# Optimization experiments

Measured on AMD Instinct MI355X. Metric: run time of the kernel, lower is better.

The kernel has to match this reference:

```python
import jax, jax.numpy as jnp
import numpy as np

B, C, H, W = 4, 96, 64, 64
N_STATE, DT_RANK, K = 16, 6, 3


def _layernorm(x, g, b, eps=1e-5):
    m = jnp.mean(x, axis=-1, keepdims=True)
    v = jnp.mean((x - m) ** 2, axis=-1, keepdims=True)
    return (x - m) / jnp.sqrt(v + eps) * g + b


def _grid_sample(img, gx, gy):
    # F.grid_sample: bilinear, align_corners=True, zeros padding; gx,gy in [-1,1], [B,Ho,Wo]
    Bc, Cc, Hi, Wi = img.shape
    fx = (gx + 1.0) * 0.5 * (Wi - 1)
    fy = (gy + 1.0) * 0.5 * (Hi - 1)
    x0 = jnp.floor(fx)
    y0 = jnp.floor(fy)
    wx1 = fx - x0
    wy1 = fy - y0

    def tap(ix, iy, w):
        valid = ((ix >= 0) & (ix < Wi) & (iy >= 0) & (iy < Hi)).astype(img.dtype)
        ic = jnp.clip(ix, 0, Wi - 1).astype(jnp.int32)
        jc = jnp.clip(iy, 0, Hi - 1).astype(jnp.int32)
        v = jax.vmap(lambda im, yy, xx: im[:, yy, xx])(img, jc, ic)  # [B,C,Ho,Wo]
        return v * (w * valid)[:, None, :, :]

    return (tap(x0, y0, (1 - wx1) * (1 - wy1)) + tap(x0 + 1, y0, wx1 * (1 - wy1))
            + tap(x0, y0 + 1, (1 - wx1) * wy1) + tap(x0 + 1, y0 + 1, wx1 * wy1))


def _resize_bilinear(img, Ho, Wo):
    # torch F.interpolate(mode='bilinear', align_corners=False)
    Bc, Cc, Hi, Wi = img.shape

    def src(n_out, n_in):
        s = jnp.maximum((jnp.arange(n_out, dtype=img.dtype) + 0.5) * (n_in / n_out) - 0.5, 0.0)
        i0 = jnp.floor(s).astype(jnp.int32)
        i1 = jnp.minimum(i0 + 1, n_in - 1)
        return i0, i1, s - i0

    y0, y1, wy = src(Ho, Hi)
    x0, x1, wx = src(Wo, Wi)
    row = img[:, :, y0, :] * (1 - wy)[None, None, :, None] + img[:, :, y1, :] * wy[None, None, :, None]
    return row[:, :, :, x0] * (1 - wx) + row[:, :, :, x1] * wx


def _conv_offset(x, conv1_w, conv1_b, ca1_w, ca1_b, ca2_w, ca2_b, ln_g, ln_b, conv2_w):
    Bc, Cc = x.shape[:2]
    p = conv1_w.shape[-1] // 2
    x1 = jax.lax.conv_general_dilated(
        x, conv1_w, (1, 1), [(p, p), (p, p)],
        dimension_numbers=("NCHW", "OIHW", "NCHW"), feature_group_count=Cc
    ) + conv1_b[None, :, None, None]
    xc = jnp.mean(x, axis=(2, 3))  # adaptive_avg_pool2d -> (1,1)
    hid = jax.nn.gelu(xc @ ca1_w.T + ca1_b, approximate=False)
    ca = jax.nn.sigmoid(hid @ ca2_w.T + ca2_b)
    x1 = x1 * ca[:, :, None, None]
    xn = _layernorm(jnp.transpose(x1, (0, 2, 3, 1)), ln_g, ln_b)
    xg = jax.nn.gelu(jnp.transpose(xn, (0, 3, 1, 2)), approximate=False)
    return jnp.einsum("bchw,oc->bohw", xg, conv2_w[:, :, 0, 0])


def _deformable(x, rpe_table, conv1_w, conv1_b, ca1_w, ca1_b, ca2_w, ca2_b, ln_g, ln_b, conv2_w):
    Bc, Cc, Hc, Wc = x.shape
    L = Hc * Wc
    off = _conv_offset(x, conv1_w, conv1_b, ca1_w, ca1_b, ca2_w, ca2_b, ln_g, ln_b, conv2_w)
    offset = off[:, :2]
    de = off[:, 2]
    rng = jnp.array([1.0 / (Hc - 1.0), 1.0 / (Wc - 1.0)], off.dtype).reshape(1, 2, 1, 1)
    offset = jnp.transpose(jnp.tanh(offset) * rng, (0, 2, 3, 1))  # [B,H,W,2] (dy,dx)
    ry = (jnp.linspace(0.5, Hc - 0.5, Hc) / (Hc - 1.0)) * 2.0 - 1.0
    rx = (jnp.linspace(0.5, Wc - 0.5, Wc) / (Wc - 1.0)) * 2.0 - 1.0
    ref = jnp.stack(jnp.meshgrid(ry, rx, indexing="ij"), -1)  # [H,W,2] (y,x)
    pos = offset + ref[None]
    de_index = jnp.tanh(de).reshape(Bc, L)
    path_ref = (jnp.linspace(0.5, L - 0.5, L) / (L - 1.0)) * 2.0 - 1.0
    path_pos = de_index + path_ref[None]
    x_sampled = _grid_sample(x, pos[..., 1], pos[..., 0])
    rpe = jnp.broadcast_to(rpe_table[None], (Bc,) + rpe_table.shape)
    rpe_bias = _resize_bilinear(rpe, Hc, Wc)
    ky = (jnp.linspace(0.0, float(Hc), Hc) / (Hc - 1.0)) * 2.0 - 1.0
    kx = (jnp.linspace(0.0, float(Wc), Wc) / (Wc - 1.0)) * 2.0 - 1.0
    key_grid = jnp.stack(jnp.meshgrid(ky, kx, indexing="ij"), -1)
    disp = (key_grid[None] - pos) * 0.5
    pos_bias = _grid_sample(rpe_bias, disp[..., 1], disp[..., 0])
    xd = (x_sampled + pos_bias).reshape(Bc, Cc, L)
    indices = jnp.argsort(path_pos, axis=-1)  # topk(k=N, largest=False) == ascending argsort
    xs2 = jnp.take_along_axis(xd, indices[:, None, :], axis=2)
    return xs2, indices


def _selective_scan(u, delta, A, Bs, Cs, Dv, delta_bias):
    Bc, KD, L = u.shape
    Kk = Bs.shape[1]
    Dd = KD // Kk
    Ns = A.shape[1]
    delta = jax.nn.softplus(delta + delta_bias[None, :, None])
    dt4 = jnp.moveaxis(delta.reshape(Bc, Kk, Dd, L), 3, 0)
    u4 = jnp.moveaxis(u.reshape(Bc, Kk, Dd, L), 3, 0)
    Bt = jnp.moveaxis(Bs, 3, 0)
    Ct = jnp.moveaxis(Cs, 3, 0)
    A3 = A.reshape(Kk, Dd, Ns)

    @jax.checkpoint
    def step(h, inp):
        dt, ut, bt, ct = inp  # [B,K,D],[B,K,D],[B,K,N],[B,K,N]
        h = jnp.exp(dt[..., None] * A3) * h + (dt * ut)[..., None] * bt[:, :, None, :]
        return h, jnp.einsum("bkdn,bkn->bkd", h, ct)

    h0 = jnp.zeros((Bc, Kk, Dd, Ns), u.dtype)
    _, ys = jax.lax.scan(step, h0, (dt4, u4, Bt, Ct))
    ys = jnp.moveaxis(ys, 0, 3).reshape(Bc, KD, L)
    return ys + u * Dv[None, :, None]


def _forward(x, x_proj_weight, dt_projs_weight, dt_projs_bias, A_logs, Ds_param,
             conv1_w, conv1_b, ca1_w, ca1_b, ca2_w, ca2_b, ln_g, ln_b, conv2_w, rpe_table):
    Bc, Dd, Hc, Wc = x.shape
    L = Hc * Wc
    Kk, _, R = dt_projs_weight.shape
    Ns = A_logs.shape[1]
    xs0 = x.reshape(Bc, Dd, L)
    xs2, indices = _deformable(x, rpe_table, conv1_w, conv1_b, ca1_w, ca1_b, ca2_w, ca2_b, ln_g, ln_b, conv2_w)
    xs = jnp.stack([xs0, xs0[..., ::-1], xs2], axis=1)  # [B,3,D,L]
    x_dbl = jnp.einsum("bkdl,kcd->bkcl", xs, x_proj_weight)
    dts, Bs, Cs = jnp.split(x_dbl, [R, R + Ns], axis=2)
    dts = jnp.einsum("bkrl,kdr->bkdl", dts, dt_projs_weight)
    A = -jnp.exp(A_logs)
    ys = _selective_scan(xs.reshape(Bc, Kk * Dd, L), dts.reshape(Bc, Kk * Dd, L),
                         A, Bs, Cs, Ds_param, dt_projs_bias.reshape(-1))
    ys = ys.reshape(Bc, Kk, Dd, L)
    inv = jnp.argsort(indices, axis=-1)  # inverse permutation (DeformableLayerReverse)
    y2 = jnp.take_along_axis(ys[:, 2], inv[:, None, :], axis=2)
    y = (ys[:, 0] + ys[:, 1][..., ::-1] + y2) / 3.0
    return jnp.transpose(y, (0, 2, 1)).reshape(Bc, Hc, Wc, Dd)


def setup_inputs():
    key = jax.random.key(0)
    ks = jax.random.split(key, 12)
    f = jnp.float32
    return {
        "x": jax.random.normal(ks[0], (B, C, H, W), f),
        "x_proj_weight": jax.random.normal(ks[1], (K, DT_RANK + 2 * N_STATE, C), f) * 0.05,
        "dt_projs_weight": jax.random.normal(ks[2], (K, C, DT_RANK), f) * 0.05,
        "dt_projs_bias": jax.random.normal(ks[3], (K, C), f) * 0.1,
        "A_logs": jnp.tile(jnp.log(jnp.arange(1, N_STATE + 1, dtype=f))[None, :], (K * C, 1)),
        "Ds_param": jnp.ones((K * C,), f),
        "conv1_w": jax.random.normal(ks[4], (C, 1, 9, 9), f) * 0.05,
        "conv1_b": jnp.zeros((C,), f),
        "ca1_w": jax.random.normal(ks[5], (C // 16, C), f) * 0.1,
        "ca1_b": jnp.zeros((C // 16,), f),
        "ca2_w": jax.random.normal(ks[6], (C, C // 16), f) * 0.1,
        "ca2_b": jnp.zeros((C,), f),
        "ln_g": jnp.ones((C,), f),
        "ln_b": jnp.zeros((C,), f),
        "conv2_w": jax.random.normal(ks[7], (3, C, 1, 1), f) * 0.05,
        "rpe_table": jax.random.normal(ks[8], (C, 7, 7), f) * 0.01,
    }


def reference(x, x_proj_weight, dt_projs_weight, dt_projs_bias, A_logs, Ds_param,
              conv1_w, conv1_b, ca1_w, ca1_b, ca2_w, ca2_b, ln_g, ln_b, conv2_w, rpe_table):
    return _forward(x, x_proj_weight, dt_projs_weight, dt_projs_bias, A_logs, Ds_param,
                    conv1_w, conv1_b, ca1_w, ca1_b, ca2_w, ca2_b, ln_g, ln_b, conv2_w, rpe_table)
```

## Files before the change

kernel.cpp:

```cpp
#include <hip/hip_runtime.h>

#define BB 4
#define CC 96
#define HH 64
#define WW 64
#define LL 4096
#define KK 3
#define RR 6
#define NN 16

__device__ __forceinline__ float geluf(float x){
    return 0.5f * x * (1.0f + erff(x * 0.70710678118654752f));
}
__device__ __forceinline__ float softplusf(float x){
    return fmaxf(x, 0.0f) + log1pf(expf(-fabsf(x)));
}
__device__ __forceinline__ float sigmoidf(float x){
    return 1.0f / (1.0f + expf(-x));
}

__global__ __launch_bounds__(256) void k_mean(const float* __restrict__ x, float* __restrict__ xc){
    int bc = blockIdx.x;
    const float* p = x + (size_t)bc * LL;
    float s = 0.f;
    for (int i = threadIdx.x; i < LL; i += 256) s += p[i];
    __shared__ float red[256];
    red[threadIdx.x] = s; __syncthreads();
    for (int st = 128; st > 0; st >>= 1){
        if (threadIdx.x < st) red[threadIdx.x] += red[threadIdx.x + st];
        __syncthreads();
    }
    if (threadIdx.x == 0) xc[bc] = red[0] * (1.0f / LL);
}

__global__ __launch_bounds__(128) void k_ca(const float* __restrict__ xc,
                     const float* __restrict__ w1, const float* __restrict__ b1,
                     const float* __restrict__ w2, const float* __restrict__ b2,
                     float* __restrict__ ca){
    int b = blockIdx.x;
    int t = threadIdx.x;
    __shared__ float hid[CC/16];
    if (t < CC/16){
        float a = b1[t];
        for (int d = 0; d < CC; d++) a += w1[t*CC + d] * xc[b*CC + d];
        hid[t] = geluf(a);
    }
    __syncthreads();
    if (t < CC){
        float a = b2[t];
        #pragma unroll
        for (int i = 0; i < CC/16; i++) a += w2[t*(CC/16) + i] * hid[i];
        ca[b*CC + t] = sigmoidf(a);
    }
}

__global__ __launch_bounds__(256) void k_conv(const float* __restrict__ x, const float* __restrict__ w,
                       const float* __restrict__ bias, const float* __restrict__ ca,
                       float* __restrict__ x1){
    int tid4 = blockIdx.x * 256 + threadIdx.x;
    int wq4 = (tid4 & 15) * 4;
    int rest = tid4 >> 4;
    int h = rest & 63;
    int bc = rest >> 6;
    int c = bc % CC; int b = bc / CC;
    const float* xp = x + (size_t)bc * LL;
    const float* wp = w + c * 81;
    float a0 = 0.f, a1 = 0.f, a2 = 0.f, a3 = 0.f;
    #pragma unroll
    for (int ky = 0; ky < 9; ky++){
        int yy = h + ky - 4;
        if (yy < 0 || yy >= HH) continue;
        const float4* row4 = (const float4*)(xp + yy*WW);
        int g = wq4 >> 2;
        float4 q0 = (wq4 >= 4)  ? row4[g-1] : make_float4(0.f,0.f,0.f,0.f);
        float4 q1 = row4[g];
        float4 q2 = (wq4 < 60)  ? row4[g+1] : make_float4(0.f,0.f,0.f,0.f);
        float v[12] = {q0.x,q0.y,q0.z,q0.w, q1.x,q1.y,q1.z,q1.w, q2.x,q2.y,q2.z,q2.w};
        const float* wr = wp + ky*9;
        #pragma unroll
        for (int kx = 0; kx < 9; kx++){
            float wk = wr[kx];
            a0 = fmaf(v[kx],   wk, a0);
            a1 = fmaf(v[kx+1], wk, a1);
            a2 = fmaf(v[kx+2], wk, a2);
            a3 = fmaf(v[kx+3], wk, a3);
        }
    }
    float sc = ca[b*CC + c];
    float bb = bias[c];
    float4 o = make_float4((a0+bb)*sc, (a1+bb)*sc, (a2+bb)*sc, (a3+bb)*sc);
    *(float4*)(x1 + (size_t)bc*LL + h*WW + wq4) = o;
}

__global__ __launch_bounds__(256) void k_rpe(const float* __restrict__ t, float* __restrict__ out){
    int gid = blockIdx.x * 256 + threadIdx.x;
    int l = gid & (LL-1); int c = gid >> 12;
    int h = l >> 6, w = l & 63;
    float sy = fmaxf((h + 0.5f) * (7.0f/64.0f) - 0.5f, 0.f);
    float sx = fmaxf((w + 0.5f) * (7.0f/64.0f) - 0.5f, 0.f);
    int y0 = (int)floorf(sy); int x0 = (int)floorf(sx);
    float wy = sy - (float)y0, wx = sx - (float)x0;
    int y1 = min(y0 + 1, 6), x1i = min(x0 + 1, 6);
    const float* tp = t + c * 49;
    float r0 = tp[y0*7 + x0] * (1.f - wy) + tp[y1*7 + x0] * wy;
    float r1 = tp[y0*7 + x1i] * (1.f - wy) + tp[y1*7 + x1i] * wy;
    out[gid] = r0 * (1.f - wx) + r1 * wx;
}

__global__ __launch_bounds__(256) void k_off(const float* __restrict__ x1,
                      const float* __restrict__ g, const float* __restrict__ bta,
                      const float* __restrict__ w2,
                      float* __restrict__ posy, float* __restrict__ posx, float* __restrict__ path){
    int blk = blockIdx.x;
    int ltile = blk & 63; int b = blk >> 6;
    int lane = threadIdx.x & 63;
    int wg = threadIdx.x >> 6;
    int l = ltile * 64 + lane;
    const float* p = x1 + (size_t)b * CC * LL + l;
    float v[24];
    float s = 0.f, ss = 0.f;
    #pragma unroll
    for (int j = 0; j < 24; j++){
        float t = p[(size_t)(wg*24 + j) * LL];
        v[j] = t; s += t; ss += t*t;
    }
    __shared__ float ls[4][64], lss[4][64];
    ls[wg][lane] = s; lss[wg][lane] = ss;
    __syncthreads();
    s  = ls[0][lane]  + ls[1][lane]  + ls[2][lane]  + ls[3][lane];
    ss = lss[0][lane] + lss[1][lane] + lss[2][lane] + lss[3][lane];
    float m = s * (1.0f/CC);
    float rstd = rsqrtf(ss*(1.0f/CC) - m*m + 1e-5f);
    float a0 = 0.f, a1 = 0.f, a2 = 0.f;
    #pragma unroll
    for (int j = 0; j < 24; j++){
        int c = wg*24 + j;
        float xn = (v[j]-m)*rstd*g[c] + bta[c];
        float xg = geluf(xn);
        a0 = fmaf(w2[c],      xg, a0);
        a1 = fmaf(w2[CC+c],   xg, a1);
        a2 = fmaf(w2[2*CC+c], xg, a2);
    }
    __shared__ float la[3][4][64];
    la[0][wg][lane] = a0; la[1][wg][lane] = a1; la[2][wg][lane] = a2;
    __syncthreads();
    if (wg < 3){
        float a = la[wg][0][lane] + la[wg][1][lane] + la[wg][2][lane] + la[wg][3][lane];
        int h = l >> 6, w = l & 63;
        if (wg == 0)      posy[b*LL + l] = tanhf(a)*(1.0f/63.0f) + ((2*h+1)*(1.0f/63.0f) - 1.0f);
        else if (wg == 1) posx[b*LL + l] = tanhf(a)*(1.0f/63.0f) + ((2*w+1)*(1.0f/63.0f) - 1.0f);
        else              path[b*LL + l] = tanhf(a) + ((l + 0.5f)*(2.0f/4095.0f) - 1.0f);
    }
}

__device__ __forceinline__ float bilin0(const float* __restrict__ img, float gx, float gy){
    float fx = (gx + 1.f) * 31.5f;
    float fy = (gy + 1.f) * 31.5f;
    float x0f = floorf(fx), y0f = floorf(fy);
    float wx = fx - x0f, wy = fy - y0f;
    int x0 = (int)x0f, y0 = (int)y0f;
    float acc = 0.f;
    bool vx0 = (x0 >= 0) & (x0 < WW), vx1 = (x0+1 >= 0) & (x0+1 < WW);
    bool vy0 = (y0 >= 0) & (y0 < HH), vy1 = (y0+1 >= 0) & (y0+1 < HH);
    if (vy0 & vx0) acc += img[y0*WW + x0]       * (1.f-wx) * (1.f-wy);
    if (vy0 & vx1) acc += img[y0*WW + x0+1]     * wx       * (1.f-wy);
    if (vy1 & vx0) acc += img[(y0+1)*WW + x0]   * (1.f-wx) * wy;
    if (vy1 & vx1) acc += img[(y0+1)*WW + x0+1] * wx       * wy;
    return acc;
}

typedef unsigned long long u64s;
__device__ __forceinline__ u64s shflx64(u64s x, int m){
    int lo = __shfl_xor((int)(unsigned)x, m);
    int hi = __shfl_xor((int)(unsigned)(x >> 32), m);
    return ((u64s)(unsigned)hi << 32) | (unsigned)lo;
}
__device__ __forceinline__ void cex(u64s& a, u64s& b, bool up){
    u64s mn = a < b ? a : b;
    u64s mx = a < b ? b : a;
    a = up ? mn : mx;
    b = up ? mx : mn;
}
__global__ __launch_bounds__(1024) void k_sortsample(
        const float* __restrict__ path, int* __restrict__ idx, int* __restrict__ inv,
        const float* __restrict__ x, const float* __restrict__ rpe,
        const float* __restrict__ posy, const float* __restrict__ posx,
        float* __restrict__ xd){
    int blk = blockIdx.x;
    if (blk < BB){
        int b = blk;
        int t = threadIdx.x;
        __shared__ u64s lds[LL];
        u64s v[4];
        #pragma unroll
        for (int r = 0; r < 4; r++){
            int e = t*4 + r;
            unsigned u = __float_as_uint(path[b*LL + e]);
            u ^= (u >> 31) ? 0xFFFFFFFFu : 0x80000000u;
            v[r] = ((u64s)u << 32) | (unsigned)e;
        }
        for (int kk = 2; kk <= LL; kk <<= 1){
            for (int j = kk >> 1; j > 0; j >>= 1){
                if (j >= 256){
                    __syncthreads();
                    #pragma unroll
                    for (int r = 0; r < 4; r++) lds[t*4 + r] = v[r];
                    __syncthreads();
                    #pragma unroll
                    for (int r = 0; r < 4; r++){
                        int e = t*4 + r;
                        u64s pv = lds[e ^ j];
                        bool up    = ((e & kk) == 0);
                        bool lower = ((e & j) == 0);
                        u64s mn = v[r] < pv ? v[r] : pv;
                        u64s mx = v[r] < pv ? pv : v[r];
                        v[r] = (up == lower) ? mn : mx;
                    }
                } else if (j >= 4){
                    int m = j >> 2;
                    #pragma unroll
                    for (int r = 0; r < 4; r++){
                        u64s pv = shflx64(v[r], m);
                        bool up    = (((t*4 + r) & kk) == 0);
                        bool lower = ((t & m) == 0);
                        u64s mn = v[r] < pv ? v[r] : pv;
                        u64s mx = v[r] < pv ? pv : v[r];
                        v[r] = (up == lower) ? mn : mx;
                    }
                } else if (j == 2){
                    bool up = (((t*4) & kk) == 0);
                    cex(v[0], v[2], up);
                    cex(v[1], v[3], up);
                } else {
                    if (kk == 2){
                        cex(v[0], v[1], true);
                        cex(v[2], v[3], false);
                    } else {
                        bool up = (((t*4) & kk) == 0);
                        cex(v[0], v[1], up);
                        cex(v[2], v[3], up);
                    }
                }
            }
        }
        #pragma unroll
        for (int r = 0; r < 4; r++){
            int e = t*4 + r;
            int id = (int)(unsigned)(v[r] & 0xFFFFFFFFu);
            idx[b*LL + e] = id;
            inv[b*LL + id] = e;
        }
    } else {
        int gid = (blk - BB) * 1024 + threadIdx.x;
        int l = gid & (LL-1); int bc = gid >> 12;
        int b = bc / CC; int c = bc % CC;
        float gy = posy[b*LL + l], gx = posx[b*LL + l];
        float v = bilin0(x + (size_t)bc * LL, gx, gy);
        int h = l >> 6, w = l & 63;
        float ky = h * (128.0f/3969.0f) - 1.0f;
        float kx = w * (128.0f/3969.0f) - 1.0f;
        float v2 = bilin0(rpe + (size_t)c * LL, (kx - gx) * 0.5f, (ky - gy) * 0.5f);
        xd[gid] = v + v2;
    }
}

__global__ __launch_bounds__(192, 1) void k_proj(const float* __restrict__ x, const float* __restrict__ xd,
    const int* __restrict__ indices, const float* __restrict__ xpw, const float* __restrict__ dtw,
    const float* __restrict__ dtb, float* __restrict__ u2, float* __restrict__ dt,
    float* __restrict__ Bst, float* __restrict__ Cst){
    int blk = blockIdx.x;
    int ltile = blk & 63; int bk = blk >> 6;
    int k = bk % KK; int b = bk / KK;
    int lane = threadIdx.x & 63;
    int w = threadIdx.x >> 6;
    const float* __restrict__ Wk = xpw + k*38*CC;
    int l = ltile * 64 + lane;
    int srcl = (k == 0) ? l : (k == 1 ? (LL-1-l) : indices[b*LL + l]);
    const float* xp = (k == 2 ? xd : x) + (size_t)b * CC * LL + srcl;

    __shared__ float vsh[CC*64];
    #pragma unroll
    for (int j = 0; j < 32; j++){
        int d = w*32 + j;
        vsh[d*64 + lane] = xp[(size_t)d * LL];
    }
    __syncthreads();

    if (w == 0){
        float acc[RR];
        #pragma unroll
        for (int i = 0; i < RR; i++) acc[i] = 0.f;
        for (int d = 0; d < CC; d++){
            float vv = vsh[d*64 + lane];
            #pragma unroll
            for (int i = 0; i < RR; i++) acc[i] = fmaf(Wk[i*CC + d], vv, acc[i]);
        }
        const float* __restrict__ Dw = dtw + k*CC*RR;
        const float* __restrict__ Db = dtb + k*CC;
        float* dtp = dt + (size_t)bk * CC * LL + l;
        #pragma unroll 8
        for (int d = 0; d < CC; d++){
            float sdt = Db[d];
            #pragma unroll
            for (int r = 0; r < RR; r++) sdt = fmaf(acc[r], Dw[d*RR + r], sdt);
            dtp[(size_t)d * LL] = softplusf(sdt);
        }
    } else if (w == 1){
        float acc[NN];
        #pragma unroll
        for (int i = 0; i < NN; i++) acc[i] = 0.f;
        for (int d = 0; d < CC; d++){
            float vv = vsh[d*64 + lane];
            #pragma unroll
            for (int i = 0; i < NN; i++) acc[i] = fmaf(Wk[(RR + i)*CC + d], vv, acc[i]);
        }
        size_t base = ((size_t)bk * LL + l) * NN;
        #pragma unroll
        for (int q = 0; q < 4; q++){
            float4 o; o.x = acc[q*4]; o.y = acc[q*4+1]; o.z = acc[q*4+2]; o.w = acc[q*4+3];
            *(float4*)(Bst + base + q*4) = o;
        }
    } else {
        float acc[NN];
        #pragma unroll
        for (int i = 0; i < NN; i++) acc[i] = 0.f;
        for (int d = 0; d < CC; d++){
            float vv = vsh[d*64 + lane];
            #pragma unroll
            for (int i = 0; i < NN; i++) acc[i] = fmaf(Wk[(RR + NN + i)*CC + d], vv, acc[i]);
        }
        size_t base = ((size_t)bk * LL + l) * NN;
        #pragma unroll
        for (int q = 0; q < 4; q++){
            float4 o; o.x = acc[q*4]; o.y = acc[q*4+1]; o.z = acc[q*4+2]; o.w = acc[q*4+3];
            *(float4*)(Cst + base + q*4) = o;
        }
        if (k == 2){
            float* up = u2 + (size_t)b * CC * LL + l;
            #pragma unroll 8
            for (int d = 0; d < CC; d++) up[(size_t)d * LL] = vsh[d*64 + lane];
        }
    }
}

#define SEG 128
#define TL 32
#define SROW 17
#define XROW 32
template<int KIND>
__device__ __forceinline__ void scan_body(int b, int d, const float* __restrict__ usrc,
    const float* __restrict__ dt, const float* __restrict__ Bst, const float* __restrict__ Cst,
    const float* __restrict__ Alog, const float* __restrict__ Ds, float* __restrict__ ys,
    float* sA, float* sB, float* sS, float* yl){
    int bk = b * KK + KIND;
    int tid = threadIdx.x;
    int ng = tid & 3;
    int seg = tid >> 2;
    int t0 = seg * TL;
    int xsw = (seg & 7) << 2;

    const float4 A4 = *(const float4*)(Alog + (KIND*CC + d)*NN + 4*ng);
    const float L2E = 1.4426950408889634f;
    float A2[4] = { -__expf(A4.x)*L2E, -__expf(A4.y)*L2E, -__expf(A4.z)*L2E, -__expf(A4.w)*L2E };
    float Dv = Ds[KIND*CC + d];

    const float* dtp = dt + ((size_t)bk * CC + d) * LL + t0;
    const float* ub = (KIND == 1)
        ? usrc + ((size_t)b*CC + d) * LL + (LL-4-t0)
        : usrc + ((size_t)b*CC + d) * LL + t0;
    const float* Bp = Bst + ((size_t)bk * LL + t0) * NN + 4*ng;
    const float* Cp = Cst + ((size_t)bk * LL + t0) * NN + 4*ng;
    float* yp = ys + ((size_t)bk * CC + d) * LL + t0;

    float h[4] = {0.f,0.f,0.f,0.f};
    float S = 0.f;
    for (int t = 0; t < TL; t += 4){
        float4 dq = *(const float4*)(dtp + t);
        float4 uq = (KIND == 1) ? *(const float4*)(ub - t) : *(const float4*)(ub + t);
        float4 Bq[4], Cq[4];
        #pragma unroll
        for (int i = 0; i < 4; i++){
            Bq[i] = *(const float4*)(Bp + (t+i)*NN);
            Cq[i] = *(const float4*)(Cp + (t+i)*NN);
        }
        float dd[4] = {dq.x, dq.y, dq.z, dq.w};
        float uu[4];
        if (KIND == 1){ uu[0]=uq.w; uu[1]=uq.z; uu[2]=uq.y; uu[3]=uq.x; }
        else          { uu[0]=uq.x; uu[1]=uq.y; uu[2]=uq.z; uu[3]=uq.w; }
        float sv[4], pv[4];
        #pragma unroll
        for (int i = 0; i < 4; i++){
            float du = dd[i] * uu[i];
            float bb[4] = {Bq[i].x, Bq[i].y, Bq[i].z, Bq[i].w};
            float cc[4] = {Cq[i].x, Cq[i].y, Cq[i].z, Cq[i].w};
            float p = 0.f;
            #pragma unroll
            for (int j = 0; j < 4; j++){
                float a = exp2f(dd[i] * A2[j]);
                h[j] = fmaf(a, h[j], du * bb[j]);
                p = fmaf(h[j], cc[j], p);
            }
            S += dd[i];
            sv[i] = S;
            p += __shfl_xor(p, 1);
            p += __shfl_xor(p, 2);
            pv[i] = fmaf(uu[i], Dv, p);
        }
        if (ng == 0){
            int xo = seg*XROW + (t ^ xsw);
            *(float4*)(sS + xo) = make_float4(sv[0], sv[1], sv[2], sv[3]);
            *(float4*)(yl + xo) = make_float4(pv[0], pv[1], pv[2], pv[3]);
        }
    }

    #pragma unroll
    for (int j = 0; j < 4; j++){
        sA[seg*SROW + 4*ng + j] = exp2f(A2[j] * S);
        sB[seg*SROW + 4*ng + j] = h[j];
    }
    __syncthreads();
    {
        int wv = tid >> 6;
        int lane = tid & 63;
        #pragma unroll
        for (int nn = 0; nn < 2; nn++){
            int n = 2*wv + nn;
            float a1 = sA[(2*lane)*SROW + n],   b1 = sB[(2*lane)*SROW + n];
            float a2 = sA[(2*lane+1)*SROW + n], b2 = sB[(2*lane+1)*SROW + n];
            float ca = a1 * a2;
            float cb = fmaf(a2, b1, b2);
            #pragma unroll
            for (int off = 1; off < 64; off <<= 1){
                float ta = __shfl_up(ca, off);
                float tb = __shfl_up(cb, off);
                if (lane >= off){
                    cb = fmaf(ca, tb, cb);
                    ca *= ta;
                }
            }
            float cb_prev = __shfl_up(cb, 1);
            if (lane == 0) cb_prev = 0.f;
            sA[(2*lane)*SROW + n]   = cb_prev;
            sA[(2*lane+1)*SROW + n] = fmaf(a1, cb_prev, b1);
        }
    }
    __syncthreads();
    float hc[4];
    #pragma unroll
    for (int j = 0; j < 4; j++) hc[j] = sA[seg*SROW + 4*ng + j];

    for (int t = 0; t < TL; t += 4){
        int xo = seg*XROW + (t ^ xsw);
        float4 sq = *(const float4*)(sS + xo);
        float4 Cq[4];
        #pragma unroll
        for (int i = 0; i < 4; i++) Cq[i] = *(const float4*)(Cp + (t+i)*NN);
        float sv[4] = {sq.x, sq.y, sq.z, sq.w};
        float yo[4];
        #pragma unroll
        for (int i = 0; i < 4; i++){
            float cc[4] = {Cq[i].x, Cq[i].y, Cq[i].z, Cq[i].w};
            float corr = 0.f;
            #pragma unroll
            for (int j = 0; j < 4; j++){
                float P = exp2f(sv[i] * A2[j]);
                corr = fmaf(P * hc[j], cc[j], corr);
            }
            corr += __shfl_xor(corr, 1);
            corr += __shfl_xor(corr, 2);
            yo[i] = corr;
        }
        if (ng == 0){
            float4 ylq = *(const float4*)(yl + xo);
            float4 o = make_float4(ylq.x + yo[0], ylq.y + yo[1], ylq.z + yo[2], ylq.w + yo[3]);
            *(float4*)(yp + t) = o;
        }
    }
}

__global__ __launch_bounds__(512) void k_scan_all(const float* __restrict__ x, const float* __restrict__ u2,
    const float* __restrict__ dt, const float* __restrict__ Bst, const float* __restrict__ Cst,
    const float* __restrict__ Alog, const float* __restrict__ Ds, float* __restrict__ ys){
    __shared__ float sA[SEG*SROW];
    __shared__ float sB[SEG*SROW];
    __shared__ float sS[SEG*XROW];
    __shared__ float yl[SEG*XROW];
    int blk = blockIdx.x;
    int k = blk / (BB*CC);
    int r = blk % (BB*CC);
    int d = r % CC; int b = r / CC;
    if (k == 0)      scan_body<0>(b, d, x,  dt, Bst, Cst, Alog, Ds, ys, sA, sB, sS, yl);
    else if (k == 1) scan_body<1>(b, d, x,  dt, Bst, Cst, Alog, Ds, ys, sA, sB, sS, yl);
    else             scan_body<2>(b, d, u2, dt, Bst, Cst, Alog, Ds, ys, sA, sB, sS, yl);
}

__global__ __launch_bounds__(256) void k_comb(const float* __restrict__ ys, const int* __restrict__ inv,
                                              float* __restrict__ out){
    int tile = blockIdx.x & 255; int b = blockIdx.x >> 8;
    int l0 = tile * 16;
    __shared__ float t0[CC * 17];
    __shared__ int invs[16];
    if (threadIdx.x < 16) invs[threadIdx.x] = inv[b*LL + l0 + threadIdx.x];
    __syncthreads();
    const float* y0p = ys + (size_t)(b*KK + 0) * CC * LL;
    const float* y1p = ys + (size_t)(b*KK + 1) * CC * LL;
    const float* y2p = ys + (size_t)(b*KK + 2) * CC * LL;
    #pragma unroll
    for (int it = 0; it < 6; it++){
        int e = it * 256 + threadIdx.x;
        int li = e & 15; int c = e >> 4;
        int l = l0 + li;
        float v = y0p[(size_t)c*LL + l] + y1p[(size_t)c*LL + (LL-1-l)] + y2p[(size_t)c*LL + invs[li]];
        t0[c*17 + li] = v * (1.0f/3.0f);
    }
    __syncthreads();
    #pragma unroll
    for (int it = 0; it < 6; it++){
        int e = it * 256 + threadIdx.x;
        int c = e % CC; int li = e / CC;
        out[((size_t)b*LL + l0 + li) * CC + c] = t0[c*17 + li];
    }
}

extern "C" void kernel_launch(void* const* d_in, const int* in_sizes, int n_in,
                              void* d_out, int out_size, void* d_ws, size_t ws_size,
                              hipStream_t stream){
    const float* x    = (const float*)d_in[0];
    const float* xpw  = (const float*)d_in[1];
    const float* dtw  = (const float*)d_in[2];
    const float* dtb  = (const float*)d_in[3];
    const float* Alog = (const float*)d_in[4];
    const float* Ds   = (const float*)d_in[5];
    const float* c1w  = (const float*)d_in[6];
    const float* c1b  = (const float*)d_in[7];
    const float* ca1w = (const float*)d_in[8];
    const float* ca1b = (const float*)d_in[9];
    const float* ca2w = (const float*)d_in[10];
    const float* ca2b = (const float*)d_in[11];
    const float* lng  = (const float*)d_in[12];
    const float* lnb  = (const float*)d_in[13];
    const float* c2w  = (const float*)d_in[14];
    const float* rpet = (const float*)d_in[15];
    float* out = (float*)d_out;

    float* ws   = (float*)d_ws;
    float* xc   = ws;
    float* ca   = xc + 384;
    float* x1   = ca + 384;
    float* rpe  = x1 + (size_t)BB*CC*LL;
    float* posy = rpe + (size_t)CC*LL;
    float* posx = posy + (size_t)BB*LL;
    float* path = posx + (size_t)BB*LL;
    float* xd   = path + (size_t)BB*LL;
    int*   idx  = (int*)(xd + (size_t)BB*CC*LL);
    int*   inv  = idx + (size_t)BB*LL;
    float* u2   = (float*)(inv + (size_t)BB*LL);
    float* dtA  = u2 + (size_t)BB*CC*LL;
    float* Bst  = dtA + (size_t)BB*KK*CC*LL;
    float* Cst  = Bst + (size_t)BB*KK*LL*NN;
    float* ysA  = Cst + (size_t)BB*KK*LL*NN;

    k_mean  <<<BB*CC, 256, 0, stream>>>(x, xc);
    k_ca    <<<BB, 128, 0, stream>>>(xc, ca1w, ca1b, ca2w, ca2b, ca);
    k_conv  <<<(BB*CC*LL/4)/256, 256, 0, stream>>>(x, c1w, c1b, ca, x1);
    k_rpe   <<<(CC*LL)/256, 256, 0, stream>>>(rpet, rpe);
    k_off   <<<BB*64, 256, 0, stream>>>(x1, lng, lnb, c2w, posy, posx, path);
    k_sortsample<<<BB + (BB*CC*LL)/1024, 1024, 0, stream>>>(path, idx, inv, x, rpe, posy, posx, xd);
    k_proj  <<<BB*KK*64, 192, 0, stream>>>(x, xd, idx, xpw, dtw, dtb, u2, dtA, Bst, Cst);
    k_scan_all<<<KK*BB*CC, 512, 0, stream>>>(x, u2, dtA, Bst, Cst, Alog, Ds, ysA);
    k_comb  <<<BB*256, 256, 0, stream>>>(ysA, inv, out);
}
```

Before: 295.8 us.

## Fuse mean with RPE resize, share x tile across two projection directions, retile offset kernel

Merges the channel-mean and RPE-table resize kernels into one launch, and splits the projection kernel so directions 0 and 1 share a single shared-memory load of x (k=1 writes reversed positions), while direction 2 runs separately after sorting. The offset kernel is retiled to 32 positions by 8 channel groups, doubling its block count. The intent is to cut launch count, redundant global reads of x, and improve occupancy of the offset stage, at the cost of longer serial work per block in the fused projection kernel.

```diff
diff --git a/kernel.cpp b/kernel.cpp
--- a/kernel.cpp
+++ b/kernel.cpp
@@ -19,18 +19,34 @@
     return 1.0f / (1.0f + expf(-x));
 }
 
-__global__ __launch_bounds__(256) void k_mean(const float* __restrict__ x, float* __restrict__ xc){
-    int bc = blockIdx.x;
-    const float* p = x + (size_t)bc * LL;
-    float s = 0.f;
-    for (int i = threadIdx.x; i < LL; i += 256) s += p[i];
-    __shared__ float red[256];
-    red[threadIdx.x] = s; __syncthreads();
-    for (int st = 128; st > 0; st >>= 1){
-        if (threadIdx.x < st) red[threadIdx.x] += red[threadIdx.x + st];
-        __syncthreads();
-    }
-    if (threadIdx.x == 0) xc[bc] = red[0] * (1.0f / LL);
+__global__ __launch_bounds__(256) void k_meanrpe(const float* __restrict__ x, float* __restrict__ xc,
+                                                 const float* __restrict__ rpet, float* __restrict__ rpe){
+    int blk = blockIdx.x;
+    if (blk < BB*CC){
+        const float* p = x + (size_t)blk * LL;
+        float s = 0.f;
+        for (int i = threadIdx.x; i < LL; i += 256) s += p[i];
+        __shared__ float red[256];
+        red[threadIdx.x] = s; __syncthreads();
+        for (int st = 128; st > 0; st >>= 1){
+            if (threadIdx.x < st) red[threadIdx.x] += red[threadIdx.x + st];
+            __syncthreads();
+        }
+        if (threadIdx.x == 0) xc[blk] = red[0] * (1.0f / LL);
+    } else {
+        int gid = (blk - BB*CC) * 256 + threadIdx.x;
+        int l = gid & (LL-1); int c = gid >> 12;
+        int h = l >> 6, w = l & 63;
+        float sy = fmaxf((h + 0.5f) * (7.0f/64.0f) - 0.5f, 0.f);
+        float sx = fmaxf((w + 0.5f) * (7.0f/64.0f) - 0.5f, 0.f);
+        int y0 = (int)floorf(sy); int x0 = (int)floorf(sx);
+        float wy = sy - (float)y0, wx = sx - (float)x0;
+        int y1 = min(y0 + 1, 6), x1i = min(x0 + 1, 6);
+        const float* tp = rpet + c * 49;
+        float r0 = tp[y0*7 + x0] * (1.f - wy) + tp[y1*7 + x0] * wy;
+        float r1 = tp[y0*7 + x1i] * (1.f - wy) + tp[y1*7 + x1i] * wy;
+        rpe[gid] = r0 * (1.f - wx) + r1 * wx;
+    }
 }
 
 __global__ __launch_bounds__(128) void k_ca(const float* __restrict__ xc,
@@ -92,63 +108,51 @@
     *(float4*)(x1 + (size_t)bc*LL + h*WW + wq4) = o;
 }
 
-__global__ __launch_bounds__(256) void k_rpe(const float* __restrict__ t, float* __restrict__ out){
-    int gid = blockIdx.x * 256 + threadIdx.x;
-    int l = gid & (LL-1); int c = gid >> 12;
-    int h = l >> 6, w = l & 63;
-    float sy = fmaxf((h + 0.5f) * (7.0f/64.0f) - 0.5f, 0.f);
-    float sx = fmaxf((w + 0.5f) * (7.0f/64.0f) - 0.5f, 0.f);
-    int y0 = (int)floorf(sy); int x0 = (int)floorf(sx);
-    float wy = sy - (float)y0, wx = sx - (float)x0;
-    int y1 = min(y0 + 1, 6), x1i = min(x0 + 1, 6);
-    const float* tp = t + c * 49;
-    float r0 = tp[y0*7 + x0] * (1.f - wy) + tp[y1*7 + x0] * wy;
-    float r1 = tp[y0*7 + x1i] * (1.f - wy) + tp[y1*7 + x1i] * wy;
-    out[gid] = r0 * (1.f - wx) + r1 * wx;
-}
-
 __global__ __launch_bounds__(256) void k_off(const float* __restrict__ x1,
                       const float* __restrict__ g, const float* __restrict__ bta,
                       const float* __restrict__ w2,
                       float* __restrict__ posy, float* __restrict__ posx, float* __restrict__ path){
     int blk = blockIdx.x;
-    int ltile = blk & 63; int b = blk >> 6;
-    int lane = threadIdx.x & 63;
-    int wg = threadIdx.x >> 6;
-    int l = ltile * 64 + lane;
+    int tile = blk & 127; int b = blk >> 7;
+    int li = threadIdx.x & 31;
+    int cg = threadIdx.x >> 5;
+    int l = tile * 32 + li;
     const float* p = x1 + (size_t)b * CC * LL + l;
-    float v[24];
+    float v[12];
     float s = 0.f, ss = 0.f;
     #pragma unroll
-    for (int j = 0; j < 24; j++){
-        float t = p[(size_t)(wg*24 + j) * LL];
+    for (int j = 0; j < 12; j++){
+        float t = p[(size_t)(cg*12 + j) * LL];
         v[j] = t; s += t; ss += t*t;
     }
-    __shared__ float ls[4][64], lss[4][64];
-    ls[wg][lane] = s; lss[wg][lane] = ss;
-    __syncthreads();
-    s  = ls[0][lane]  + ls[1][lane]  + ls[2][lane]  + ls[3][lane];
-    ss = lss[0][lane] + lss[1][lane] + lss[2][lane] + lss[3][lane];
+    __shared__ float ls[8][32], lss[8][32];
+    ls[cg][li] = s; lss[cg][li] = ss;
+    __syncthreads();
+    s = 0.f; ss = 0.f;
+    #pragma unroll
+    for (int g2 = 0; g2 < 8; g2++){ s += ls[g2][li]; ss += lss[g2][li]; }
     float m = s * (1.0f/CC);
     float rstd = rsqrtf(ss*(1.0f/CC) - m*m + 1e-5f);
     float a0 = 0.f, a1 = 0.f, a2 = 0.f;
     #pragma unroll
-    for (int j = 0; j < 24; j++){
-        int c = wg*24 + j;
+    for (int j = 0; j < 12; j++){
+        int c = cg*12 + j;
         float xn = (v[j]-m)*rstd*g[c] + bta[c];
         float xg = geluf(xn);
         a0 = fmaf(w2[c],      xg, a0);
         a1 = fmaf(w2[CC+c],   xg, a1);
         a2 = fmaf(w2[2*CC+c], xg, a2);
     }
-    __shared__ float la[3][4][64];
-    la[0][wg][lane] = a0; la[1][wg][lane] = a1; la[2][wg][lane] = a2;
-    __syncthreads();
-    if (wg < 3){
-        float a = la[wg][0][lane] + la[wg][1][lane] + la[wg][2][lane] + la[wg][3][lane];
-        int h = l >> 6, w = l & 63;
-        if (wg == 0)      posy[b*LL + l] = tanhf(a)*(1.0f/63.0f) + ((2*h+1)*(1.0f/63.0f) - 1.0f);
-        else if (wg == 1) posx[b*LL + l] = tanhf(a)*(1.0f/63.0f) + ((2*w+1)*(1.0f/63.0f) - 1.0f);
+    __shared__ float la[3][8][32];
+    la[0][cg][li] = a0; la[1][cg][li] = a1; la[2][cg][li] = a2;
+    __syncthreads();
+    if (cg < 3){
+        float a = 0.f;
+        #pragma unroll
+        for (int g2 = 0; g2 < 8; g2++) a += la[cg][g2][li];
+        int h = l >> 6, ww = l & 63;
+        if (cg == 0)      posy[b*LL + l] = tanhf(a)*(1.0f/63.0f) + ((2*h+1)*(1.0f/63.0f) - 1.0f);
+        else if (cg == 1) posx[b*LL + l] = tanhf(a)*(1.0f/63.0f) + ((2*ww+1)*(1.0f/63.0f) - 1.0f);
         else              path[b*LL + l] = tanhf(a) + ((l + 0.5f)*(2.0f/4095.0f) - 1.0f);
     }
 }
@@ -264,19 +268,96 @@
     }
 }
 
-__global__ __launch_bounds__(192, 1) void k_proj(const float* __restrict__ x, const float* __restrict__ xd,
+__global__ __launch_bounds__(192, 1) void k_proj01(const float* __restrict__ x,
+    const float* __restrict__ xpw, const float* __restrict__ dtw,
+    const float* __restrict__ dtb, float* __restrict__ dt,
+    float* __restrict__ Bst, float* __restrict__ Cst){
+    int blk = blockIdx.x;
+    int ltile = blk & 63; int b = blk >> 6;
+    int lane = threadIdx.x & 63;
+    int w = threadIdx.x >> 6;
+    int l = ltile * 64 + lane;
+    const float* xp = x + (size_t)b * CC * LL + l;
+
+    __shared__ float vsh[CC*64];
+    #pragma unroll
+    for (int j = 0; j < 32; j++){
+        int d = w*32 + j;
+        vsh[d*64 + lane] = xp[(size_t)d * LL];
+    }
+    __syncthreads();
+
+    #pragma unroll
+    for (int kk = 0; kk < 2; kk++){
+        const float* __restrict__ Wk = xpw + kk*38*CC;
+        int bk = b * KK + kk;
+        int lk = (kk == 0) ? l : (LL-1-l);
+        if (w == 0){
+            float acc[RR];
+            #pragma unroll
+            for (int i = 0; i < RR; i++) acc[i] = 0.f;
+            for (int d = 0; d < CC; d++){
+                float vv = vsh[d*64 + lane];
+                #pragma unroll
+                for (int i = 0; i < RR; i++) acc[i] = fmaf(Wk[i*CC + d], vv, acc[i]);
+            }
+            const float* __restrict__ Dw = dtw + kk*CC*RR;
+            const float* __restrict__ Db = dtb + kk*CC;
+            float* dtp = dt + (size_t)bk * CC * LL + lk;
+            #pragma unroll 8
+            for (int d = 0; d < CC; d++){
+                float sdt = Db[d];
+                #pragma unroll
+                for (int r = 0; r < RR; r++) sdt = fmaf(acc[r], Dw[d*RR + r], sdt);
+                dtp[(size_t)d * LL] = softplusf(sdt);
+            }
+        } else if (w == 1){
+            float acc[NN];
+            #pragma unroll
+            for (int i = 0; i < NN; i++) acc[i] = 0.f;
+            for (int d = 0; d < CC; d++){
+                float vv = vsh[d*64 + lane];
+                #pragma unroll
+                for (int i = 0; i < NN; i++) acc[i] = fmaf(Wk[(RR + i)*CC + d], vv, acc[i]);
+            }
+            size_t base = ((size_t)bk * LL + lk) * NN;
+            #pragma unroll
+            for (int q = 0; q < 4; q++){
+                float4 o; o.x = acc[q*4]; o.y = acc[q*4+1]; o.z = acc[q*4+2]; o.w = acc[q*4+3];
+                *(float4*)(Bst + base + q*4) = o;
+            }
+        } else {
+            float acc[NN];
+            #pragma unroll
+            for (int i = 0; i < NN; i++) acc[i] = 0.f;
+            for (int d = 0; d < CC; d++){
+                float vv = vsh[d*64 + lane];
+                #pragma unroll
+                for (int i = 0; i < NN; i++) acc[i] = fmaf(Wk[(RR + NN + i)*CC + d], vv, acc[i]);
+            }
+            size_t base = ((size_t)bk * LL + lk) * NN;
+            #pragma unroll
+            for (int q = 0; q < 4; q++){
+                float4 o; o.x = acc[q*4]; o.y = acc[q*4+1]; o.z = acc[q*4+2]; o.w = acc[q*4+3];
+                *(float4*)(Cst + base + q*4) = o;
+            }
+        }
+    }
+}
+
+__global__ __launch_bounds__(192, 1) void k_proj2(const float* __restrict__ xd,
     const int* __restrict__ indices, const float* __restrict__ xpw, const float* __restrict__ dtw,
     const float* __restrict__ dtb, float* __restrict__ u2, float* __restrict__ dt,
     float* __restrict__ Bst, float* __restrict__ Cst){
     int blk = blockIdx.x;
-    int ltile = blk & 63; int bk = blk >> 6;
-    int k = bk % KK; int b = bk / KK;
+    int ltile = blk & 63; int b = blk >> 6;
     int lane = threadIdx.x & 63;
     int w = threadIdx.x >> 6;
-    const float* __restrict__ Wk = xpw + k*38*CC;
+    const float* __restrict__ Wk = xpw + 2*38*CC;
+    int bk = b * KK + 2;
     int l = ltile * 64 + lane;
-    int srcl = (k == 0) ? l : (k == 1 ? (LL-1-l) : indices[b*LL + l]);
-    const float* xp = (k == 2 ? xd : x) + (size_t)b * CC * LL + srcl;
+    int srcl = indices[b*LL + l];
+    const float* xp = xd + (size_t)b * CC * LL + srcl;
 
     __shared__ float vsh[CC*64];
     #pragma unroll
@@ -295,8 +376,8 @@
             #pragma unroll
             for (int i = 0; i < RR; i++) acc[i] = fmaf(Wk[i*CC + d], vv, acc[i]);
         }
-        const float* __restrict__ Dw = dtw + k*CC*RR;
-        const float* __restrict__ Db = dtb + k*CC;
+        const float* __restrict__ Dw = dtw + 2*CC*RR;
+        const float* __restrict__ Db = dtb + 2*CC;
         float* dtp = dt + (size_t)bk * CC * LL + l;
         #pragma unroll 8
         for (int d = 0; d < CC; d++){
@@ -335,11 +416,9 @@
             float4 o; o.x = acc[q*4]; o.y = acc[q*4+1]; o.z = acc[q*4+2]; o.w = acc[q*4+3];
             *(float4*)(Cst + base + q*4) = o;
         }
-        if (k == 2){
-            float* up = u2 + (size_t)b * CC * LL + l;
-            #pragma unroll 8
-            for (int d = 0; d < CC; d++) up[(size_t)d * LL] = vsh[d*64 + lane];
-        }
+        float* up = u2 + (size_t)b * CC * LL + l;
+        #pragma unroll 8
+        for (int d = 0; d < CC; d++) up[(size_t)d * LL] = vsh[d*64 + lane];
     }
 }
 
@@ -560,13 +639,13 @@
     float* Cst  = Bst + (size_t)BB*KK*LL*NN;
     float* ysA  = Cst + (size_t)BB*KK*LL*NN;
 
-    k_mean  <<<BB*CC, 256, 0, stream>>>(x, xc);
-    k_ca    <<<BB, 128, 0, stream>>>(xc, ca1w, ca1b, ca2w, ca2b, ca);
-    k_conv  <<<(BB*CC*LL/4)/256, 256, 0, stream>>>(x, c1w, c1b, ca, x1);
-    k_rpe   <<<(CC*LL)/256, 256, 0, stream>>>(rpet, rpe);
-    k_off   <<<BB*64, 256, 0, stream>>>(x1, lng, lnb, c2w, posy, posx, path);
+    k_meanrpe  <<<BB*CC + (CC*LL)/256, 256, 0, stream>>>(x, xc, rpet, rpe);
+    k_ca       <<<BB, 128, 0, stream>>>(xc, ca1w, ca1b, ca2w, ca2b, ca);
+    k_proj01   <<<BB*64, 192, 0, stream>>>(x, xpw, dtw, dtb, dtA, Bst, Cst);
+    k_conv     <<<(BB*CC*LL/4)/256, 256, 0, stream>>>(x, c1w, c1b, ca, x1);
+    k_off      <<<BB*128, 256, 0, stream>>>(x1, lng, lnb, c2w, posy, posx, path);
     k_sortsample<<<BB + (BB*CC*LL)/1024, 1024, 0, stream>>>(path, idx, inv, x, rpe, posy, posx, xd);
-    k_proj  <<<BB*KK*64, 192, 0, stream>>>(x, xd, idx, xpw, dtw, dtb, u2, dtA, Bst, Cst);
-    k_scan_all<<<KK*BB*CC, 512, 0, stream>>>(x, u2, dtA, Bst, Cst, Alog, Ds, ysA);
-    k_comb  <<<BB*256, 256, 0, stream>>>(ysA, inv, out);
-}
+    k_proj2    <<<BB*64, 192, 0, stream>>>(xd, idx, xpw, dtw, dtb, u2, dtA, Bst, Cst);
+    k_scan_all <<<KK*BB*CC, 512, 0, stream>>>(x, u2, dtA, Bst, Cst, Alog, Ds, ysA);
+    k_comb     <<<BB*256, 256, 0, stream>>>(ysA, inv, out);
+}
```

Measured after the change: 399.6 us. +35.1%, slower.
